# Kernel tuning notes

Hardware: AMD Instinct MI355X
Metric: run time of the kernel (lower is better)

Reference implementation:

```python
import jax, jax.numpy as jnp
import numpy as np

N_QUBITS = 4
N_LAYERS = 6
NUM_CLASSES = 10


def _apply_1q(state, gate, wire):
    # state: (B,2,2,2,2); gate: (2,2) shared or (B,2,2) per-sample
    s = jnp.moveaxis(state, wire + 1, -1)
    if gate.ndim == 3:
        s = jnp.einsum('bij,b...j->b...i', gate, s)
    else:
        s = jnp.einsum('ij,b...j->b...i', gate, s)
    return jnp.moveaxis(s, -1, wire + 1)


def _apply_cnot(state, c, t):
    s = jnp.moveaxis(state, (c + 1, t + 1), (-2, -1))
    s = jnp.stack([s[..., 0, :], s[..., 1, ::-1]], axis=-2)
    return jnp.moveaxis(s, (-2, -1), (c + 1, t + 1))


def _rot(phi, theta, omega):
    # PennyLane Rot = RZ(omega) @ RY(theta) @ RZ(phi)
    c, s = jnp.cos(theta / 2), jnp.sin(theta / 2)
    ep = jnp.exp(-0.5j * (phi + omega))
    em = jnp.exp(-0.5j * (phi - omega))
    return jnp.stack([
        jnp.stack([ep * c, -jnp.conj(em) * s]),
        jnp.stack([em * s, jnp.conj(ep) * c]),
    ])


def _quantum_net(angles, q_weights):
    # batched default.qubit statevector simulation, 4 wires
    B = angles.shape[0]
    state = jnp.zeros((B, 2, 2, 2, 2), jnp.complex64).at[:, 0, 0, 0, 0].set(1.0)
    # AngleEmbedding, rotation='Y' (per-sample RY gates)
    for w in range(N_QUBITS):
        a = angles[:, w]
        c, s = jnp.cos(a / 2), jnp.sin(a / 2)
        g = jnp.stack([jnp.stack([c, -s], -1), jnp.stack([s, c], -1)], -2)
        state = _apply_1q(state, g.astype(jnp.complex64), w)
    # StronglyEntanglingLayers: Rot on each wire, then ring of CNOTs with range r
    for l in range(N_LAYERS):
        for w in range(N_QUBITS):
            state = _apply_1q(state, _rot(q_weights[l, w, 0], q_weights[l, w, 1], q_weights[l, w, 2]), w)
        r = l % (N_QUBITS - 1) + 1
        for w in range(N_QUBITS):
            state = _apply_cnot(state, w, (w + r) % N_QUBITS)
    probs = jnp.abs(state) ** 2  # (B,2,2,2,2)
    z = jnp.array([1.0, -1.0], dtype=probs.dtype)
    exps = [jnp.einsum('bijkl,' + 'ijkl'[w] + '->b', probs, z) for w in range(N_QUBITS)]
    return jnp.stack(exps, -1)  # (B,4) expval PauliZ per wire


def setup_inputs() -> dict:
    key = jax.random.key(0)
    ks = jax.random.split(key, 6)
    B = 65536
    x = jax.random.normal(ks[0], (B, 512), jnp.float32)
    W_pre = jax.random.normal(ks[1], (N_QUBITS, 512), jnp.float32) / np.sqrt(512)
    b_pre = jax.random.normal(ks[2], (N_QUBITS,), jnp.float32) * 0.01
    q_weights = 0.01 * jax.random.normal(ks[3], (N_LAYERS, N_QUBITS, 3), jnp.float32)
    W_post = jax.random.normal(ks[4], (NUM_CLASSES, N_QUBITS), jnp.float32) / np.sqrt(N_QUBITS)
    b_post = jax.random.normal(ks[5], (NUM_CLASSES,), jnp.float32) * 0.01
    return {'x': x, 'W_pre': W_pre, 'b_pre': b_pre, 'q_weights': q_weights,
            'W_post': W_post, 'b_post': b_post}


def reference(x, W_pre, b_pre, q_weights, W_post, b_post):
    pre = x @ W_pre.T + b_pre                 # (B,4)
    angles = jnp.tanh(pre) * np.float32(np.pi)
    q_out = _quantum_net(angles, q_weights)   # (B,4)
    return q_out @ W_post.T + b_post          # (B,10)
```

## Files before the change

kernel.cpp:

```cpp
#include <hip/hip_runtime.h>
#include <math.h>

#define BLOCK 128
#define ROWS_PER_BLOCK 128
#define K 512
#define K4 128
#define NQ 4
#define NL 6
#define NC 10

__global__ __launch_bounds__(BLOCK) void vqc_fused_kernel(
    const float* __restrict__ x,
    const float* __restrict__ W_pre,
    const float* __restrict__ b_pre,
    const float* __restrict__ q_weights,
    const float* __restrict__ W_post,
    const float* __restrict__ b_post,
    float* __restrict__ out)
{
    __shared__ float Ws[NQ * K];
    __shared__ float gates[NL * NQ][8];
    __shared__ float angles_s[ROWS_PER_BLOCK][NQ];
    __shared__ float Wpost_s[NC * NQ];
    __shared__ float bpost_s[NC];
    __shared__ float bpre_s[NQ];

    const int tid = threadIdx.x;

    {
        const float4* src = (const float4*)W_pre;
        float4* dst = (float4*)Ws;
        #pragma unroll
        for (int i = 0; i < (NQ * K4) / BLOCK; ++i)
            dst[tid + i * BLOCK] = src[tid + i * BLOCK];
    }
    if (tid < NL * NQ) {
        const int l = tid >> 2, w = tid & 3;
        const float phi = q_weights[l * 12 + w * 3 + 0];
        const float th  = q_weights[l * 12 + w * 3 + 1];
        const float om  = q_weights[l * 12 + w * 3 + 2];
        const float c  = cosf(0.5f * th), s = sinf(0.5f * th);
        const float hp = 0.5f * (phi + om), hm = 0.5f * (phi - om);
        const float epr = cosf(hp), epi = -sinf(hp);
        const float emr = cosf(hm), emi = -sinf(hm);
        gates[tid][0] =  epr * c;  gates[tid][1] =  epi * c;
        gates[tid][2] = -emr * s;  gates[tid][3] =  emi * s;
        gates[tid][4] =  emr * s;  gates[tid][5] =  emi * s;
        gates[tid][6] =  epr * c;  gates[tid][7] = -epi * c;
    }
    if (tid >= 64 && tid < 64 + NC * NQ) Wpost_s[tid - 64] = W_post[tid - 64];
    if (tid >= 104 && tid < 104 + NC)    bpost_s[tid - 104] = b_post[tid - 104];
    if (tid >= 114 && tid < 114 + NQ)    bpre_s[tid - 114]  = b_pre[tid - 114];
    __syncthreads();

    const int j = tid & 3;
    const int g = tid >> 2;
    const int rowBase = blockIdx.x * ROWS_PER_BLOCK;
    const float4* x4  = (const float4*)x;
    const float4* Ws4 = (const float4*)Ws;

    for (int s = 0; s < ROWS_PER_BLOCK / 32; ++s) {
        const int rl = s * 32 + g;
        const int r  = rowBase + rl;
        const float4* xrow = x4 + (size_t)r * K4;
        float acc0 = 0.f, acc1 = 0.f, acc2 = 0.f, acc3 = 0.f;
        #pragma unroll 8
        for (int it = 0; it < 32; ++it) {
            const int f4 = it * 4 + j;
            const float4 xv = xrow[f4];
            const float4 w0 = Ws4[0 * K4 + f4];
            const float4 w1 = Ws4[1 * K4 + f4];
            const float4 w2 = Ws4[2 * K4 + f4];
            const float4 w3 = Ws4[3 * K4 + f4];
            acc0 += xv.x * w0.x + xv.y * w0.y + xv.z * w0.z + xv.w * w0.w;
            acc1 += xv.x * w1.x + xv.y * w1.y + xv.z * w1.z + xv.w * w1.w;
            acc2 += xv.x * w2.x + xv.y * w2.y + xv.z * w2.z + xv.w * w2.w;
            acc3 += xv.x * w3.x + xv.y * w3.y + xv.z * w3.z + xv.w * w3.w;
        }
        acc0 += __shfl_xor(acc0, 1); acc0 += __shfl_xor(acc0, 2);
        acc1 += __shfl_xor(acc1, 1); acc1 += __shfl_xor(acc1, 2);
        acc2 += __shfl_xor(acc2, 1); acc2 += __shfl_xor(acc2, 2);
        acc3 += __shfl_xor(acc3, 1); acc3 += __shfl_xor(acc3, 2);
        const float accj = (j == 0) ? acc0 : (j == 1) ? acc1 : (j == 2) ? acc2 : acc3;
        angles_s[rl][j] = tanhf(accj + bpre_s[j]) * 3.14159265358979323846f;
    }
    __syncthreads();

    {
        const int rl = tid;
        const int r  = rowBase + rl;
        const float a0 = angles_s[rl][0], a1 = angles_s[rl][1];
        const float a2 = angles_s[rl][2], a3 = angles_s[rl][3];
        float c0, s0, c1, s1, c2, s2, c3, s3;
        __sincosf(0.5f * a0, &s0, &c0);
        __sincosf(0.5f * a1, &s1, &c1);
        __sincosf(0.5f * a2, &s2, &c2);
        __sincosf(0.5f * a3, &s3, &c3);

        float ar[16], ai[16];
        #pragma unroll
        for (int i = 0; i < 16; ++i) {
            ar[i] = ((i & 8) ? s0 : c0) * ((i & 4) ? s1 : c1)
                  * ((i & 2) ? s2 : c2) * ((i & 1) ? s3 : c3);
            ai[i] = 0.f;
        }

        #pragma unroll
        for (int l = 0; l < NL; ++l) {
            #pragma unroll
            for (int w = 0; w < NQ; ++w) {
                const float* G = gates[l * 4 + w];
                const float g00r = G[0], g00i = G[1], g01r = G[2], g01i = G[3];
                const float g10r = G[4], g10i = G[5], g11r = G[6], g11i = G[7];
                const int m = 8 >> w;
                #pragma unroll
                for (int i0 = 0; i0 < 16; ++i0) {
                    if (i0 & m) continue;
                    const int i1 = i0 | m;
                    const float A0r = ar[i0], A0i = ai[i0];
                    const float A1r = ar[i1], A1i = ai[i1];
                    ar[i0] = g00r * A0r - g00i * A0i + g01r * A1r - g01i * A1i;
                    ai[i0] = g00r * A0i + g00i * A0r + g01r * A1i + g01i * A1r;
                    ar[i1] = g10r * A0r - g10i * A0i + g11r * A1r - g11i * A1i;
                    ai[i1] = g10r * A0i + g10i * A0r + g11r * A1i + g11i * A1r;
                }
            }
            const int rr = l % 3 + 1;
            #pragma unroll
            for (int w = 0; w < NQ; ++w) {
                const int cm = 8 >> w;
                const int tm = 8 >> ((w + rr) & 3);
                #pragma unroll
                for (int i = 0; i < 16; ++i) {
                    if ((i & cm) && !(i & tm)) {
                        const int ii = i | tm;
                        float t;
                        t = ar[i]; ar[i] = ar[ii]; ar[ii] = t;
                        t = ai[i]; ai[i] = ai[ii]; ai[ii] = t;
                    }
                }
            }
        }

        float e0 = 0.f, e1 = 0.f, e2 = 0.f, e3 = 0.f;
        #pragma unroll
        for (int i = 0; i < 16; ++i) {
            const float p = ar[i] * ar[i] + ai[i] * ai[i];
            e0 += (i & 8) ? -p : p;
            e1 += (i & 4) ? -p : p;
            e2 += (i & 2) ? -p : p;
            e3 += (i & 1) ? -p : p;
        }

        float* orow = out + (size_t)r * NC;
        #pragma unroll
        for (int c = 0; c < NC; ++c) {
            orow[c] = bpost_s[c]
                    + Wpost_s[c * 4 + 0] * e0 + Wpost_s[c * 4 + 1] * e1
                    + Wpost_s[c * 4 + 2] * e2 + Wpost_s[c * 4 + 3] * e3;
        }
    }
}

extern "C" void kernel_launch(void* const* d_in, const int* in_sizes, int n_in,
                              void* d_out, int out_size, void* d_ws, size_t ws_size,
                              hipStream_t stream) {
    const float* x         = (const float*)d_in[0];
    const float* W_pre     = (const float*)d_in[1];
    const float* b_pre     = (const float*)d_in[2];
    const float* q_weights = (const float*)d_in[3];
    const float* W_post    = (const float*)d_in[4];
    const float* b_post    = (const float*)d_in[5];
    float* out = (float*)d_out;

    const int B = in_sizes[0] / K;
    dim3 grid(B / ROWS_PER_BLOCK);
    vqc_fused_kernel<<<grid, BLOCK, 0, stream>>>(x, W_pre, b_pre, q_weights,
                                                 W_post, b_post, out);
}
```

Before: 244.1 us.

## Use one wave per row with register-held W_pre and smaller blocks

Each 64-lane wave now processes whole rows, with every lane loading two float4s of the row and holding its slice of W_pre in registers. A full-wave xor-shuffle reduction replaces the 4-lane partial sums and the shared-memory copy of W_pre. Blocks become 256 threads covering 32 rows, which gives four times as many blocks for the same batch. The aim is better memory-level parallelism and occupancy on the bandwidth-bound x read, at the cost of a 6-step shuffle reduction per row and only 32 of 256 threads doing the statevector simulation.

```diff
diff --git a/kernel.cpp b/kernel.cpp
--- a/kernel.cpp
+++ b/kernel.cpp
@@ -1,15 +1,17 @@
 #include <hip/hip_runtime.h>
 #include <math.h>
 
-#define BLOCK 128
-#define ROWS_PER_BLOCK 128
+#define BLOCK 256
+#define WAVES_PER_BLOCK 4
+#define ROWS_PER_WAVE 8
+#define ROWS_PER_BLOCK 32
 #define K 512
 #define K4 128
 #define NQ 4
 #define NL 6
 #define NC 10
 
-__global__ __launch_bounds__(BLOCK) void vqc_fused_kernel(
+__global__ __launch_bounds__(BLOCK, 4) void vqc_fused_kernel(
     const float* __restrict__ x,
     const float* __restrict__ W_pre,
     const float* __restrict__ b_pre,
@@ -18,22 +20,16 @@
     const float* __restrict__ b_post,
     float* __restrict__ out)
 {
-    __shared__ float Ws[NQ * K];
     __shared__ float gates[NL * NQ][8];
     __shared__ float angles_s[ROWS_PER_BLOCK][NQ];
     __shared__ float Wpost_s[NC * NQ];
     __shared__ float bpost_s[NC];
     __shared__ float bpre_s[NQ];
 
-    const int tid = threadIdx.x;
+    const int tid  = threadIdx.x;
+    const int wave = tid >> 6;
+    const int lane = tid & 63;
 
-    {
-        const float4* src = (const float4*)W_pre;
-        float4* dst = (float4*)Ws;
-        #pragma unroll
-        for (int i = 0; i < (NQ * K4) / BLOCK; ++i)
-            dst[tid + i * BLOCK] = src[tid + i * BLOCK];
-    }
     if (tid < NL * NQ) {
         const int l = tid >> 2, w = tid & 3;
         const float phi = q_weights[l * 12 + w * 3 + 0];
@@ -53,42 +49,48 @@
     if (tid >= 114 && tid < 114 + NQ)    bpre_s[tid - 114]  = b_pre[tid - 114];
     __syncthreads();
 
-    const int j = tid & 3;
-    const int g = tid >> 2;
-    const int rowBase = blockIdx.x * ROWS_PER_BLOCK;
-    const float4* x4  = (const float4*)x;
-    const float4* Ws4 = (const float4*)Ws;
+    const float4* x4 = (const float4*)x;
+    const float4* W4 = (const float4*)W_pre;
+    const float4 w0a = W4[0 * K4 + lane], w0b = W4[0 * K4 + 64 + lane];
+    const float4 w1a = W4[1 * K4 + lane], w1b = W4[1 * K4 + 64 + lane];
+    const float4 w2a = W4[2 * K4 + lane], w2b = W4[2 * K4 + 64 + lane];
+    const float4 w3a = W4[3 * K4 + lane], w3b = W4[3 * K4 + 64 + lane];
 
-    for (int s = 0; s < ROWS_PER_BLOCK / 32; ++s) {
-        const int rl = s * 32 + g;
-        const int r  = rowBase + rl;
+    const int rowBase = blockIdx.x * ROWS_PER_BLOCK + wave * ROWS_PER_WAVE;
+
+    #pragma unroll 4
+    for (int rr = 0; rr < ROWS_PER_WAVE; ++rr) {
+        const int r = rowBase + rr;
         const float4* xrow = x4 + (size_t)r * K4;
-        float acc0 = 0.f, acc1 = 0.f, acc2 = 0.f, acc3 = 0.f;
-        #pragma unroll 8
-        for (int it = 0; it < 32; ++it) {
-            const int f4 = it * 4 + j;
-            const float4 xv = xrow[f4];
-            const float4 w0 = Ws4[0 * K4 + f4];
-            const float4 w1 = Ws4[1 * K4 + f4];
-            const float4 w2 = Ws4[2 * K4 + f4];
-            const float4 w3 = Ws4[3 * K4 + f4];
-            acc0 += xv.x * w0.x + xv.y * w0.y + xv.z * w0.z + xv.w * w0.w;
-            acc1 += xv.x * w1.x + xv.y * w1.y + xv.z * w1.z + xv.w * w1.w;
-            acc2 += xv.x * w2.x + xv.y * w2.y + xv.z * w2.z + xv.w * w2.w;
-            acc3 += xv.x * w3.x + xv.y * w3.y + xv.z * w3.z + xv.w * w3.w;
+        const float4 xa = xrow[lane];
+        const float4 xb = xrow[64 + lane];
+        float acc0 = xa.x * w0a.x + xa.y * w0a.y + xa.z * w0a.z + xa.w * w0a.w
+                   + xb.x * w0b.x + xb.y * w0b.y + xb.z * w0b.z + xb.w * w0b.w;
+        float acc1 = xa.x * w1a.x + xa.y * w1a.y + xa.z * w1a.z + xa.w * w1a.w
+                   + xb.x * w1b.x + xb.y * w1b.y + xb.z * w1b.z + xb.w * w1b.w;
+        float acc2 = xa.x * w2a.x + xa.y * w2a.y + xa.z * w2a.z + xa.w * w2a.w
+                   + xb.x * w2b.x + xb.y * w2b.y + xb.z * w2b.z + xb.w * w2b.w;
+        float acc3 = xa.x * w3a.x + xa.y * w3a.y + xa.z * w3a.z + xa.w * w3a.w
+                   + xb.x * w3b.x + xb.y * w3b.y + xb.z * w3b.z + xb.w * w3b.w;
+        #pragma unroll
+        for (int m = 1; m < 64; m <<= 1) {
+            acc0 += __shfl_xor(acc0, m);
+            acc1 += __shfl_xor(acc1, m);
+            acc2 += __shfl_xor(acc2, m);
+            acc3 += __shfl_xor(acc3, m);
         }
-        acc0 += __shfl_xor(acc0, 1); acc0 += __shfl_xor(acc0, 2);
-        acc1 += __shfl_xor(acc1, 1); acc1 += __shfl_xor(acc1, 2);
-        acc2 += __shfl_xor(acc2, 1); acc2 += __shfl_xor(acc2, 2);
-        acc3 += __shfl_xor(acc3, 1); acc3 += __shfl_xor(acc3, 2);
-        const float accj = (j == 0) ? acc0 : (j == 1) ? acc1 : (j == 2) ? acc2 : acc3;
-        angles_s[rl][j] = tanhf(accj + bpre_s[j]) * 3.14159265358979323846f;
+        if (lane < NQ) {
+            const float accj = (lane == 0) ? acc0 : (lane == 1) ? acc1
+                             : (lane == 2) ? acc2 : acc3;
+            angles_s[wave * ROWS_PER_WAVE + rr][lane] =
+                tanhf(accj + bpre_s[lane]) * 3.14159265358979323846f;
+        }
     }
     __syncthreads();
 
-    {
+    if (tid < ROWS_PER_BLOCK) {
         const int rl = tid;
-        const int r  = rowBase + rl;
+        const int r  = blockIdx.x * ROWS_PER_BLOCK + rl;
         const float a0 = angles_s[rl][0], a1 = angles_s[rl][1];
         const float a2 = angles_s[rl][2], a3 = angles_s[rl][3];
         float c0, s0, c1, s1, c2, s2, c3, s3;
@@ -125,11 +127,11 @@
                     ai[i1] = g10r * A0i + g10i * A0r + g11r * A1i + g11i * A1r;
                 }
             }
-            const int rr = l % 3 + 1;
+            const int rshift = l % 3 + 1;
             #pragma unroll
             for (int w = 0; w < NQ; ++w) {
                 const int cm = 8 >> w;
-                const int tm = 8 >> ((w + rr) & 3);
+                const int tm = 8 >> ((w + rshift) & 3);
                 #pragma unroll
                 for (int i = 0; i < 16; ++i) {
                     if ((i & cm) && !(i & tm)) {
```

Result: faster. 214.9 us (-11.9%).
